# Performance work log

Measured on AMD Instinct MI355X. Metric: run time of the kernel, lower is better.

## Reference

```python
import jax, jax.numpy as jnp
import numpy as np

EMBED = 768
HEADS = 12
HEAD_DIM = EMBED // HEADS
HIDDEN = 4 * EMBED


def layer_norm(x, gamma, beta, eps=1e-5):
    mu = jnp.mean(x, axis=-1, keepdims=True)
    var = jnp.var(x, axis=-1, keepdims=True)
    return (x - mu) * jax.lax.rsqrt(var + eps) * gamma + beta


def setup_inputs() -> dict:
    key = jax.random.key(0)
    ks = jax.random.split(key, 10)
    B, N, C = 64, 577, EMBED
    s_in = 1.0 / np.sqrt(C)
    s_hid = 1.0 / np.sqrt(HIDDEN)
    return {
        "x": jax.random.normal(ks[0], (B, N, C), jnp.float32),
        "ln1_g": jnp.ones((C,), jnp.float32),
        "ln1_b": jnp.zeros((C,), jnp.float32),
        "w_qkv": jax.random.normal(ks[1], (C, 3 * C), jnp.float32) * s_in,  # no bias (qkv_bias=False)
        "w_proj": jax.random.normal(ks[2], (C, C), jnp.float32) * s_in,
        "b_proj": jnp.zeros((C,), jnp.float32),
        "ln2_g": jnp.ones((C,), jnp.float32),
        "ln2_b": jnp.zeros((C,), jnp.float32),
        "w_fc1": jax.random.normal(ks[3], (C, HIDDEN), jnp.float32) * s_in,
        "b_fc1": jnp.zeros((HIDDEN,), jnp.float32),
        "w_fc2": jax.random.normal(ks[4], (HIDDEN, C), jnp.float32) * s_hid,
        "b_fc2": jnp.zeros((C,), jnp.float32),
    }


def reference(x, ln1_g, ln1_b, w_qkv, w_proj, b_proj, ln2_g, ln2_b, w_fc1, b_fc1, w_fc2, b_fc2):
    B, N, C = x.shape
    # --- attention branch (pre-norm) ---
    h = layer_norm(x, ln1_g, ln1_b)
    qkv = (h @ w_qkv).reshape(B, N, 3, HEADS, HEAD_DIM)
    q = jnp.transpose(qkv[:, :, 0], (0, 2, 1, 3))  # [B,H,N,D]
    k = jnp.transpose(qkv[:, :, 1], (0, 2, 1, 3))
    v = jnp.transpose(qkv[:, :, 2], (0, 2, 1, 3))
    scale = HEAD_DIM ** -0.5
    att = jax.nn.softmax(jnp.einsum("bhnd,bhmd->bhnm", q, k) * scale, axis=-1)
    o = jnp.einsum("bhnm,bhmd->bhnd", att, v)
    o = jnp.transpose(o, (0, 2, 1, 3)).reshape(B, N, C)
    x = x + (o @ w_proj + b_proj)
    # --- MLP branch (pre-norm) ---
    h = layer_norm(x, ln2_g, ln2_b)
    h = jax.nn.gelu(h @ w_fc1 + b_fc1, approximate=False)
    x = x + (h @ w_fc2 + b_fc2)
    return x
```

## Files before the change

kernel.cpp:

```cpp
#include <hip/hip_runtime.h>
#include <hip/hip_bf16.h>
#include <math.h>

using bf16 = __hip_bfloat16;
typedef __attribute__((ext_vector_type(8))) short short8;
typedef __attribute__((ext_vector_type(4))) float f32x4;

#define NSEQ   577
#define NBATCH 64
#define NTOK   36928
#define MPAD   37120
#define NHEADS 12
#define HDIM   64
#define NP     640
#define CEMB   768
#define CHID   3072
#define NBH    (NBATCH*NHEADS)

__device__ __forceinline__ bf16 f2bf(float v){ return __float2bfloat16(v); }

__device__ __forceinline__ float gelu_f(float x) {
    float x3 = x * x * x;
    float y = 1.5957691216057308f * (x + 0.044715f * x3);
    float e = __expf(y);
    float t = 1.0f - 2.0f / (e + 1.0f);
    return 0.5f * x * (1.0f + t);
}

#define GLOAD_LDS16(gaddr, laddr) \
  __builtin_amdgcn_global_load_lds((__attribute__((address_space(1))) const void*)(gaddr), \
                                   (__attribute__((address_space(3))) void*)(laddr), 16, 0, 0)

__global__ __launch_bounds__(256) void transpose_w(const float* __restrict__ src,
                                                   bf16* __restrict__ dst, int R, int C) {
    long idx = (long)blockIdx.x * 256 + threadIdx.x;
    long total = (long)R * C;
    if (idx < total) {
        int r = (int)(idx / C);
        int c = (int)(idx - (long)r * C);
        dst[(long)c * R + r] = f2bf(src[idx]);
    }
}

__global__ __launch_bounds__(256) void ln_kernel(const float* __restrict__ x,
                                                 const float* __restrict__ gamma,
                                                 const float* __restrict__ beta,
                                                 bf16* __restrict__ out) {
    int row = blockIdx.x;
    const float* xr = x + (size_t)row * CEMB;
    int tid = threadIdx.x;
    float v0 = xr[tid], v1 = xr[tid + 256], v2 = xr[tid + 512];
    float s = v0 + v1 + v2;
    #pragma unroll
    for (int o = 32; o > 0; o >>= 1) s += __shfl_down(s, o);
    __shared__ float red[4];
    if ((tid & 63) == 0) red[tid >> 6] = s;
    __syncthreads();
    float mean = (red[0] + red[1] + red[2] + red[3]) * (1.0f / CEMB);
    float d0 = v0 - mean, d1 = v1 - mean, d2 = v2 - mean;
    float q = d0*d0 + d1*d1 + d2*d2;
    #pragma unroll
    for (int o = 32; o > 0; o >>= 1) q += __shfl_down(q, o);
    __shared__ float red2[4];
    if ((tid & 63) == 0) red2[tid >> 6] = q;
    __syncthreads();
    float var = (red2[0] + red2[1] + red2[2] + red2[3]) * (1.0f / CEMB);
    float rs = rsqrtf(var + 1e-5f);
    bf16* orow = out + (size_t)row * CEMB;
    orow[tid]       = f2bf(d0 * rs * gamma[tid]       + beta[tid]);
    orow[tid + 256] = f2bf(d1 * rs * gamma[tid + 256] + beta[tid + 256]);
    orow[tid + 512] = f2bf(d2 * rs * gamma[tid + 512] + beta[tid + 512]);
}

__global__ __launch_bounds__(256) void flash_attn(const bf16* __restrict__ qg,
                                                  const bf16* __restrict__ kg,
                                                  const bf16* __restrict__ vtg,
                                                  bf16* __restrict__ og) {
    const int tid = threadIdx.x, lane = tid & 63, w = tid >> 6;
    const int fr = lane & 15, fh = lane >> 4;
    const int bh = blockIdx.y;
    const int q0 = blockIdx.x * 128;
    const int wr = w * 32;

    __shared__ bf16 Ks[2][64 * 64];
    __shared__ bf16 Vs[2][64 * 64];
    __shared__ bf16 Ps[128 * 64];

    const bf16* qb = qg  + (size_t)bh * NP * HDIM;
    const bf16* kb = kg  + (size_t)bh * NP * HDIM;
    const bf16* vb = vtg + (size_t)bh * HDIM * NP;

    const int swz  = (fr & 7) << 3;
    const int scol = (((lane & 7) ^ (lane >> 3)) << 3);
    const int srow = lane >> 3;

    short8 qa[2][2];
    #pragma unroll
    for (int mi = 0; mi < 2; mi++)
        #pragma unroll
        for (int ks = 0; ks < 2; ks++)
            qa[mi][ks] = *reinterpret_cast<const short8*>(
                qb + (size_t)(q0 + wr + mi * 16 + fr) * HDIM + ks * 32 + fh * 8);
    #pragma unroll
    for (int mi = 0; mi < 2; mi++)
        #pragma unroll
        for (int ks = 0; ks < 2; ks++)
            asm volatile("" : "+v"(qa[mi][ks]));

    f32x4 od[2][4] = {};
    float m_run[2] = {-1e30f, -1e30f};
    float l_run[2] = {0.f, 0.f};

    auto stageKV = [&](int buf, int kb0) {
        GLOAD_LDS16(kb + (size_t)(kb0 + w * 8 + srow) * HDIM + scol,      Ks[buf] + w * 512);
        GLOAD_LDS16(kb + (size_t)(kb0 + 32 + w * 8 + srow) * HDIM + scol, Ks[buf] + 2048 + w * 512);
        GLOAD_LDS16(vb + (size_t)(w * 8 + srow) * NP + kb0 + scol,        Vs[buf] + w * 512);
        GLOAD_LDS16(vb + (size_t)(32 + w * 8 + srow) * NP + kb0 + scol,   Vs[buf] + 2048 + w * 512);
    };

    auto tileBody = [&](int buf, int kb0) {
        f32x4 sacc[2][4] = {};
        short8 kf[4][2];
        #pragma unroll
        for (int n = 0; n < 4; n++)
            #pragma unroll
            for (int ks = 0; ks < 2; ks++)
                kf[n][ks] = *reinterpret_cast<const short8*>(
                    &Ks[buf][(n * 16 + fr) * 64 + ((ks * 32 + fh * 8) ^ swz)]);
        __builtin_amdgcn_s_setprio(1);
        #pragma unroll
        for (int mi = 0; mi < 2; mi++)
            #pragma unroll
            for (int n = 0; n < 4; n++)
                #pragma unroll
                for (int ks = 0; ks < 2; ks++)
                    sacc[mi][n] = __builtin_amdgcn_mfma_f32_16x16x32_bf16(kf[n][ks], qa[mi][ks], sacc[mi][n], 0, 0, 0);
        __builtin_amdgcn_s_setprio(0);

        #pragma unroll
        for (int mi = 0; mi < 2; mi++) {
            float sv[4][4];
            float tm = -1e30f;
            #pragma unroll
            for (int n = 0; n < 4; n++)
                #pragma unroll
                for (int r = 0; r < 4; r++) {
                    int key = kb0 + n * 16 + fh * 4 + r;
                    float s = sacc[mi][n][r];
                    sv[n][r] = (key < NSEQ) ? s : -1e30f;
                    tm = fmaxf(tm, sv[n][r]);
                }
            tm = fmaxf(tm, __shfl_xor(tm, 16));
            tm = fmaxf(tm, __shfl_xor(tm, 32));
            float mo = m_run[mi];
            if (__any(tm - mo > 8.f)) {
                float mn = fmaxf(mo, tm);
                float sc = __expf(mo - mn);
                m_run[mi] = mn;
                l_run[mi] *= sc;
                #pragma unroll
                for (int r = 0; r < 4; r++) {
                    float s2 = __shfl(sc, fh * 4 + r);
                    #pragma unroll
                    for (int n2 = 0; n2 < 4; n2++) od[mi][n2][r] *= s2;
                }
                mo = mn;
            }
            float ps = 0.f;
            #pragma unroll
            for (int n = 0; n < 4; n++)
                #pragma unroll
                for (int r = 0; r < 4; r++) {
                    float e = __expf(sv[n][r] - mo);
                    sv[n][r] = e; ps += e;
                }
            ps += __shfl_xor(ps, 16);
            ps += __shfl_xor(ps, 32);
            l_run[mi] += ps;
            const int q = wr + mi * 16 + fr;
            char* prow = (char*)(Ps + q * 64);
            #pragma unroll
            for (int n = 0; n < 4; n++) {
                bf16 b0 = f2bf(sv[n][0]), b1 = f2bf(sv[n][1]);
                bf16 b2 = f2bf(sv[n][2]), b3 = f2bf(sv[n][3]);
                unsigned int lo = (unsigned int)*(unsigned short*)&b0 |
                                  ((unsigned int)*(unsigned short*)&b1 << 16);
                unsigned int hi = (unsigned int)*(unsigned short*)&b2 |
                                  ((unsigned int)*(unsigned short*)&b3 << 16);
                int chunk = (2 * n + (fh >> 1)) ^ (fr & 7);
                uint2 pk; pk.x = lo; pk.y = hi;
                *reinterpret_cast<uint2*>(prow + (chunk << 4) + ((fh & 1) << 3)) = pk;
            }
        }
        asm volatile("s_waitcnt lgkmcnt(0)" ::: "memory");
        __builtin_amdgcn_sched_barrier(0);

        short8 pa[2][2], vf[4][2];
        #pragma unroll
        for (int mi = 0; mi < 2; mi++)
            #pragma unroll
            for (int ks = 0; ks < 2; ks++)
                pa[mi][ks] = *reinterpret_cast<const short8*>(
                    &Ps[(wr + mi * 16 + fr) * 64 + ((ks * 32 + fh * 8) ^ swz)]);
        #pragma unroll
        for (int n2 = 0; n2 < 4; n2++)
            #pragma unroll
            for (int ks = 0; ks < 2; ks++)
                vf[n2][ks] = *reinterpret_cast<const short8*>(
                    &Vs[buf][(n2 * 16 + fr) * 64 + ((ks * 32 + fh * 8) ^ swz)]);
        __builtin_amdgcn_s_setprio(1);
        #pragma unroll
        for (int mi = 0; mi < 2; mi++)
            #pragma unroll
            for (int n2 = 0; n2 < 4; n2++)
                #pragma unroll
                for (int ks = 0; ks < 2; ks++)
                    od[mi][n2] = __builtin_amdgcn_mfma_f32_16x16x32_bf16(pa[mi][ks], vf[n2][ks], od[mi][n2], 0, 0, 0);
        __builtin_amdgcn_s_setprio(0);
    };

    stageKV(0, 0);
    stageKV(1, 64);
    for (int t = 0; t < 9; ++t) {
        asm volatile("s_waitcnt vmcnt(4)" ::: "memory");
        __builtin_amdgcn_s_barrier();
        tileBody(t & 1, t * 64);
        asm volatile("s_waitcnt lgkmcnt(0)" ::: "memory");
        __builtin_amdgcn_s_barrier();
        if (t + 2 < 10) stageKV(t & 1, (t + 2) * 64);
    }
    asm volatile("s_waitcnt vmcnt(0)" ::: "memory");
    __builtin_amdgcn_s_barrier();
    tileBody(1, 9 * 64);

    const int b = bh / NHEADS, hh = bh - b * NHEADS;
    #pragma unroll
    for (int mi = 0; mi < 2; mi++)
        #pragma unroll
        for (int r = 0; r < 4; r++) {
            float lv = __shfl(l_run[mi], fh * 4 + r);
            int qrow = q0 + wr + mi * 16 + fh * 4 + r;
            if (qrow < NSEQ) {
                float inv = 1.f / lv;
                #pragma unroll
                for (int n2 = 0; n2 < 4; n2++)
                    og[((size_t)(b * NSEQ + qrow)) * CEMB + hh * HDIM + n2 * 16 + fr] =
                        f2bf(od[mi][n2][r] * inv);
            }
        }
}

#define MODE_QKV  1
#define MODE_PROJ 3
#define MODE_FC1  4
#define MODE_FC2  5

struct GemmParams {
    const bf16* A;
    const bf16* Bt;
    int M, N, K;
    int Mreal;
    float* Cf;
    bf16* Cb;
    const float* bias;
    const float* resid;
    bf16* qb; bf16* kb; bf16* vtb;
};

template<int MODE>
__global__ __launch_bounds__(512, 2) void gemm256(GemmParams p) {
    __shared__ bf16 AsBuf[2][256 * 64];
    __shared__ bf16 BsBuf[2][256 * 64];
    const int tid  = threadIdx.x;
    const int lane = tid & 63;
    const int w    = tid >> 6;

    const int gx = gridDim.x, gy = gridDim.y;
    const int nwg = gx * gy;
    const int orig = blockIdx.y * gx + blockIdx.x;
    const int q8 = nwg >> 3, r8 = nwg & 7;
    const int xcd = orig & 7, oid = orig >> 3;
    const int lin2 = ((xcd < r8) ? xcd * (q8 + 1) : r8 * (q8 + 1) + (xcd - r8) * q8) + oid;
    const int bm = (lin2 / gy) * 256;
    const int bn = (lin2 % gy) * 256;

    const int Kd = p.K;
    const int wm = w >> 2, wn = w & 3;
    const int wr = wm * 128, wc = wn * 64;
    const int fr = lane & 15;
    const int fk = (lane >> 4) * 8;
    const int swz = (fr & 7) << 3;

    const int sr = w * 8 + (lane >> 3);
    const int scol = (((lane & 7) ^ (lane >> 3)) << 3);
    const bf16* aS[4]; const bf16* bS[4];
    #pragma unroll
    for (int s = 0; s < 4; s++) {
        aS[s] = p.A  + (size_t)(bm + s * 64 + sr) * Kd + scol;
        bS[s] = p.Bt + (size_t)(bn + s * 64 + sr) * Kd + scol;
    }

    f32x4 acc[8][4] = {};

    auto stage = [&](bf16* Ad, bf16* Bd) {
        #pragma unroll
        for (int s = 0; s < 4; s++) {
            GLOAD_LDS16(aS[s], Ad + (size_t)(s * 8 + w) * 512);
            GLOAD_LDS16(bS[s], Bd + (size_t)(s * 8 + w) * 512);
            aS[s] += 64; bS[s] += 64;
        }
    };
    auto compute = [&](const bf16* Ad, const bf16* Bd) {
        #pragma unroll
        for (int ks = 0; ks < 2; ks++) {
            short8 b[4];
            #pragma unroll
            for (int n = 0; n < 4; n++)
                b[n] = *reinterpret_cast<const short8*>(
                    &Bd[(wc + n * 16 + fr) * 64 + ((ks * 32 + fk) ^ swz)]);
            #pragma unroll
            for (int m = 0; m < 8; m++) {
                short8 a = *reinterpret_cast<const short8*>(
                    &Ad[(wr + m * 16 + fr) * 64 + ((ks * 32 + fk) ^ swz)]);
                #pragma unroll
                for (int n = 0; n < 4; n++)
                    acc[m][n] = __builtin_amdgcn_mfma_f32_16x16x32_bf16(a, b[n], acc[m][n], 0, 0, 0);
            }
        }
    };

    const int T = Kd >> 6;
    stage(AsBuf[0], BsBuf[0]);
    __syncthreads();
    for (int t = 1; t < T; ++t) {
        stage(AsBuf[t & 1], BsBuf[t & 1]);
        compute(AsBuf[(t - 1) & 1], BsBuf[(t - 1) & 1]);
        __syncthreads();
    }
    compute(AsBuf[(T - 1) & 1], BsBuf[(T - 1) & 1]);

    const int fq = (lane >> 4) * 4;
    const int colw = bn + wc;

    if (MODE == MODE_QKV) {
        const int which = colw / CEMB;
        const int hh = (colw - which * CEMB) >> 6;
        const float scl = (which == 0) ? 0.125f : 1.0f;
        #pragma unroll
        for (int m = 0; m < 8; m++)
        #pragma unroll
        for (int r = 0; r < 4; r++) {
            int row = bm + wr + m * 16 + fq + r;
            if (row < p.Mreal) {
                int b2 = row / NSEQ;
                int n2 = row - b2 * NSEQ;
                size_t bh = (size_t)b2 * NHEADS + hh;
                if (which == 0) {
                    bf16* dst = p.qb + (bh * NP + n2) * HDIM + fr;
                    #pragma unroll
                    for (int n = 0; n < 4; n++) dst[n * 16] = f2bf(acc[m][n][r] * scl);
                } else if (which == 1) {
                    bf16* dst = p.kb + (bh * NP + n2) * HDIM + fr;
                    #pragma unroll
                    for (int n = 0; n < 4; n++) dst[n * 16] = f2bf(acc[m][n][r]);
                } else {
                    bf16* dst = p.vtb + (bh * HDIM + fr) * NP + n2;
                    #pragma unroll
                    for (int n = 0; n < 4; n++) dst[(size_t)n * 16 * NP] = f2bf(acc[m][n][r]);
                }
            }
        }
    } else if (MODE == MODE_FC1) {
        const float* bp = p.bias + colw + fr;
        float bb[4];
        #pragma unroll
        for (int n = 0; n < 4; n++) bb[n] = bp[n * 16];
        #pragma unroll
        for (int m = 0; m < 8; m++)
        #pragma unroll
        for (int r = 0; r < 4; r++) {
            int row = bm + wr + m * 16 + fq + r;
            if (row < p.Mreal) {
                bf16* crow = p.Cb + (size_t)row * p.N + colw + fr;
                #pragma unroll
                for (int n = 0; n < 4; n++)
                    crow[n * 16] = f2bf(gelu_f(acc[m][n][r] + bb[n]));
            }
        }
    } else {
        const float* bp = p.bias + colw + fr;
        float bb[4];
        #pragma unroll
        for (int n = 0; n < 4; n++) bb[n] = bp[n * 16];
        #pragma unroll
        for (int m = 0; m < 8; m++)
        #pragma unroll
        for (int r = 0; r < 4; r++) {
            int row = bm + wr + m * 16 + fq + r;
            if (row < p.Mreal) {
                float* crow = p.Cf + (size_t)row * p.N + colw + fr;
                const float* rrow = p.resid + (size_t)row * p.N + colw + fr;
                #pragma unroll
                for (int n = 0; n < 4; n++)
                    crow[n * 16] = acc[m][n][r] + bb[n] + rrow[n * 16];
            }
        }
    }
}

extern "C" void kernel_launch(void* const* d_in, const int* in_sizes, int n_in,
                              void* d_out, int out_size, void* d_ws, size_t ws_size,
                              hipStream_t stream) {
    const float* x      = (const float*)d_in[0];
    const float* ln1_g  = (const float*)d_in[1];
    const float* ln1_b  = (const float*)d_in[2];
    const float* w_qkv  = (const float*)d_in[3];
    const float* w_proj = (const float*)d_in[4];
    const float* b_proj = (const float*)d_in[5];
    const float* ln2_g  = (const float*)d_in[6];
    const float* ln2_b  = (const float*)d_in[7];
    const float* w_fc1  = (const float*)d_in[8];
    const float* b_fc1  = (const float*)d_in[9];
    const float* w_fc2  = (const float*)d_in[10];
    const float* b_fc2  = (const float*)d_in[11];
    float* out = (float*)d_out;

    char* ws = (char*)d_ws;
    auto al = [](size_t b){ return (b + 255) & ~(size_t)255; };
    size_t off = 0;
    auto take = [&](size_t b)->char* { char* p = ws + off; off += al(b); return p; };

    bf16* wqkvT  = (bf16*)take((size_t)2304 * 768 * 2);
    bf16* wprojT = (bf16*)take((size_t)768 * 768 * 2);
    bf16* wfc1T  = (bf16*)take((size_t)3072 * 768 * 2);
    bf16* wfc2T  = (bf16*)take((size_t)768 * 3072 * 2);
    bf16* h      = (bf16*)take((size_t)MPAD * CEMB * 2);
    bf16* o      = (bf16*)take((size_t)MPAD * CEMB * 2);
    size_t fixedEnd = off;

    const size_t qkvB = (size_t)NBH * NP * HDIM * 2;
    bf16* q_c  = (bf16*)(ws + fixedEnd);
    bf16* k_c  = (bf16*)(ws + fixedEnd + qkvB);
    bf16* vT_c = (bf16*)(ws + fixedEnd + 2 * qkvB);
    bf16* g_c  = (bf16*)(ws + fixedEnd);

    transpose_w<<<(768 * 2304 + 255) / 256, 256, 0, stream>>>(w_qkv, wqkvT, 768, 2304);
    transpose_w<<<(768 * 768 + 255) / 256, 256, 0, stream>>>(w_proj, wprojT, 768, 768);
    transpose_w<<<(768 * 3072 + 255) / 256, 256, 0, stream>>>(w_fc1, wfc1T, 768, 3072);
    transpose_w<<<(3072 * 768 + 255) / 256, 256, 0, stream>>>(w_fc2, wfc2T, 3072, 768);

    ln_kernel<<<NTOK, 256, 0, stream>>>(x, ln1_g, ln1_b, h);

    {
        GemmParams p{};
        p.A = h; p.Bt = wqkvT;
        p.M = MPAD; p.N = 3 * CEMB; p.K = CEMB; p.Mreal = NTOK;
        p.qb = q_c; p.kb = k_c; p.vtb = vT_c;
        gemm256<MODE_QKV><<<dim3(MPAD / 256, 3 * CEMB / 256), 512, 0, stream>>>(p);
    }

    flash_attn<<<dim3(NP / 128, NBH), 256, 0, stream>>>(q_c, k_c, vT_c, o);

    {
        GemmParams p{};
        p.A = o; p.Bt = wprojT;
        p.M = MPAD; p.N = CEMB; p.K = CEMB; p.Mreal = NTOK;
        p.Cf = out; p.bias = b_proj; p.resid = x;
        gemm256<MODE_PROJ><<<dim3(MPAD / 256, CEMB / 256), 512, 0, stream>>>(p);
    }

    ln_kernel<<<NTOK, 256, 0, stream>>>(out, ln2_g, ln2_b, h);

    {
        GemmParams p{};
        p.A = h; p.Bt = wfc1T;
        p.M = MPAD; p.N = CHID; p.K = CEMB; p.Mreal = NTOK;
        p.Cb = g_c; p.bias = b_fc1;
        gemm256<MODE_FC1><<<dim3(MPAD / 256, CHID / 256), 512, 0, stream>>>(p);
    }

    {
        GemmParams p{};
        p.A = g_c; p.Bt = wfc2T;
        p.M = MPAD; p.N = CEMB; p.K = CHID; p.Mreal = NTOK;
        p.Cf = out; p.bias = b_fc2; p.resid = out;
        gemm256<MODE_FC2><<<dim3(MPAD / 256, CEMB / 256), 512, 0, stream>>>(p);
    }
}
```

Measured before the change: 1.302 ms.

## Restructure GEMM main loop into interleaved phases with staged loads and priority

```diff
diff --git a/kernel.cpp b/kernel.cpp
--- a/kernel.cpp
+++ b/kernel.cpp
@@ -293,51 +293,61 @@
 
     const int sr = w * 8 + (lane >> 3);
     const int scol = (((lane & 7) ^ (lane >> 3)) << 3);
-    const bf16* aS[4]; const bf16* bS[4];
-    #pragma unroll
-    for (int s = 0; s < 4; s++) {
-        aS[s] = p.A  + (size_t)(bm + s * 64 + sr) * Kd + scol;
-        bS[s] = p.Bt + (size_t)(bn + s * 64 + sr) * Kd + scol;
-    }
 
     f32x4 acc[8][4] = {};
 
-    auto stage = [&](bf16* Ad, bf16* Bd) {
-        #pragma unroll
-        for (int s = 0; s < 4; s++) {
-            GLOAD_LDS16(aS[s], Ad + (size_t)(s * 8 + w) * 512);
-            GLOAD_LDS16(bS[s], Bd + (size_t)(s * 8 + w) * 512);
-            aS[s] += 64; bS[s] += 64;
-        }
+    auto stageS = [&](bf16* Ad, bf16* Bd, int kt, int s) {
+        GLOAD_LDS16(p.A  + (size_t)(bm + s * 64 + sr) * Kd + (size_t)kt * 64 + scol,
+                    Ad + (size_t)(s * 8 + w) * 512);
+        GLOAD_LDS16(p.Bt + (size_t)(bn + s * 64 + sr) * Kd + (size_t)kt * 64 + scol,
+                    Bd + (size_t)(s * 8 + w) * 512);
     };
-    auto compute = [&](const bf16* Ad, const bf16* Bd) {
-        #pragma unroll
-        for (int ks = 0; ks < 2; ks++) {
-            short8 b[4];
+
+    auto PHASE = [&](const bf16* Ad, const bf16* Bd, int ks, int mh,
+                     bf16* An, bf16* Bn, int ktn, int s0, int s1, bool doStage) {
+        short8 bfr[4], afr[4];
+        #pragma unroll
+        for (int n = 0; n < 4; n++)
+            bfr[n] = *reinterpret_cast<const short8*>(
+                &Bd[(wc + n * 16 + fr) * 64 + ((ks * 32 + fk) ^ swz)]);
+        #pragma unroll
+        for (int m = 0; m < 4; m++)
+            afr[m] = *reinterpret_cast<const short8*>(
+                &Ad[(wr + (mh * 4 + m) * 16 + fr) * 64 + ((ks * 32 + fk) ^ swz)]);
+        if (doStage) { stageS(An, Bn, ktn, s0); stageS(An, Bn, ktn, s1); }
+        __builtin_amdgcn_s_barrier();
+        asm volatile("s_waitcnt lgkmcnt(0)" ::: "memory");
+        __builtin_amdgcn_sched_barrier(0);
+        __builtin_amdgcn_s_setprio(1);
+        #pragma unroll
+        for (int m = 0; m < 4; m++)
             #pragma unroll
             for (int n = 0; n < 4; n++)
-                b[n] = *reinterpret_cast<const short8*>(
-                    &Bd[(wc + n * 16 + fr) * 64 + ((ks * 32 + fk) ^ swz)]);
-            #pragma unroll
-            for (int m = 0; m < 8; m++) {
-                short8 a = *reinterpret_cast<const short8*>(
-                    &Ad[(wr + m * 16 + fr) * 64 + ((ks * 32 + fk) ^ swz)]);
-                #pragma unroll
-                for (int n = 0; n < 4; n++)
-                    acc[m][n] = __builtin_amdgcn_mfma_f32_16x16x32_bf16(a, b[n], acc[m][n], 0, 0, 0);
-            }
-        }
+                acc[mh * 4 + m][n] = __builtin_amdgcn_mfma_f32_16x16x32_bf16(
+                    afr[m], bfr[n], acc[mh * 4 + m][n], 0, 0, 0);
+        __builtin_amdgcn_s_setprio(0);
+        __builtin_amdgcn_s_barrier();
     };
 
     const int T = Kd >> 6;
-    stage(AsBuf[0], BsBuf[0]);
-    __syncthreads();
-    for (int t = 1; t < T; ++t) {
-        stage(AsBuf[t & 1], BsBuf[t & 1]);
-        compute(AsBuf[(t - 1) & 1], BsBuf[(t - 1) & 1]);
-        __syncthreads();
-    }
-    compute(AsBuf[(T - 1) & 1], BsBuf[(T - 1) & 1]);
+    stageS(AsBuf[0], BsBuf[0], 0, 0);
+    stageS(AsBuf[0], BsBuf[0], 0, 1);
+    stageS(AsBuf[0], BsBuf[0], 0, 2);
+    stageS(AsBuf[0], BsBuf[0], 0, 3);
+    asm volatile("s_waitcnt vmcnt(0)" ::: "memory");
+    __builtin_amdgcn_s_barrier();
+
+    for (int t = 0; t < T; ++t) {
+        const bf16* Ad = AsBuf[t & 1]; const bf16* Bd = BsBuf[t & 1];
+        bf16* An = AsBuf[(t + 1) & 1]; bf16* Bn = BsBuf[(t + 1) & 1];
+        const bool st = (t + 1 < T);
+        PHASE(Ad, Bd, 0, 0, An, Bn, t + 1, 0, 1, st);
+        PHASE(Ad, Bd, 0, 1, An, Bn, t + 1, 2, 3, st);
+        PHASE(Ad, Bd, 1, 0, An, Bn, 0, 0, 0, false);
+        PHASE(Ad, Bd, 1, 1, An, Bn, 0, 0, 0, false);
+        if (st) asm volatile("s_waitcnt vmcnt(0)" ::: "memory");
+        __builtin_amdgcn_s_barrier();
+    }
 
     const int fq = (lane >> 4) * 4;
     const int colw = bn + wc;
```

Result: slower. 1.349 ms (+3.6%).
